# Performance work log

Hardware: AMD Instinct MI355X
Metric: run time of the kernel (lower is better)

Reference implementation:

```python
import jax, jax.numpy as jnp
import numpy as np

N = 50000       # nodes
E = 800000      # raw edges (self-loops added in reference, per PyG GATConv default)
F_IN = 256      # input feature dim (dataset.num_features stand-in)
H = 4           # heads (layer 1)
C = 32          # hidden_channels per head
CLS = 16        # num_classes (layer 2 out, heads=1)


def setup_inputs() -> dict:
    key = jax.random.key(0)
    ks = jax.random.split(key, 12)
    s = 0.05
    return {
        "x": jax.random.normal(ks[0], (N, F_IN), jnp.float32),
        "edge_index": jax.random.randint(ks[1], (2, E), 0, N, dtype=jnp.int64),
        "W1": jax.random.normal(ks[2], (F_IN, H * C), jnp.float32) * s,
        "att_src1": jax.random.normal(ks[3], (H, C), jnp.float32) * s,
        "att_dst1": jax.random.normal(ks[4], (H, C), jnp.float32) * s,
        "b1": jnp.zeros((H * C,), jnp.float32),
        "W2": jax.random.normal(ks[5], (H * C, CLS), jnp.float32) * s,
        "att_src2": jax.random.normal(ks[6], (1, CLS), jnp.float32) * s,
        "att_dst2": jax.random.normal(ks[7], (1, CLS), jnp.float32) * s,
        "b2": jnp.zeros((CLS,), jnp.float32),
    }


def gat_conv(x, src, dst, W, a_src, a_dst, b, heads, ch):
    """One GATConv (concat=True). src/dst include self-loops."""
    n = x.shape[0]
    h = (x @ W).reshape(n, heads, ch)                       # [N,H,C]
    alpha_s = jnp.sum(h * a_src, axis=-1)                   # [N,H]
    alpha_d = jnp.sum(h * a_dst, axis=-1)                   # [N,H]
    e = jax.nn.leaky_relu(alpha_s[src] + alpha_d[dst], 0.2) # [E',H]
    # segment softmax over incoming edges of each destination node
    m = jax.ops.segment_max(e, dst, num_segments=n)         # [N,H]
    ex = jnp.exp(e - m[dst])
    den = jax.ops.segment_sum(ex, dst, num_segments=n)      # [N,H]
    coef = ex / (den[dst] + 1e-16)                          # [E',H]
    # weighted scatter-aggregate of source features
    out = jax.ops.segment_sum(h[src] * coef[:, :, None], dst, num_segments=n)
    return out.reshape(n, heads * ch) + b


def reference(x, edge_index, W1, att_src1, att_dst1, b1, W2, att_src2, att_dst2, b2):
    n = x.shape[0]
    loop = jnp.arange(n, dtype=edge_index.dtype)
    src = jnp.concatenate([edge_index[0], loop])
    dst = jnp.concatenate([edge_index[1], loop])
    # eval mode: F.dropout is identity
    h = gat_conv(x, src, dst, W1, att_src1, att_dst1, b1, H, C)
    h = jax.nn.elu(h)
    out = gat_conv(h, src, dst, W2, att_src2, att_dst2, b2, 1, CLS)
    return out
```

## Files before the change

### kernel.cpp

```cpp
#include <hip/hip_runtime.h>
#include <hip/hip_bf16.h>
#include <math.h>

#define NNODES 50000
#define FIN 256
#define HH 4
#define CC 32
#define D1 128
#define CLS 16
#define NBUCK ((NNODES + 255) >> 8)
#define CHUNK 4096

typedef __attribute__((ext_vector_type(8))) short bfrag8;
typedef __attribute__((ext_vector_type(4))) float facc4;

__device__ __forceinline__ float lrelu(float x){ return x > 0.f ? x : 0.2f*x; }

__device__ __forceinline__ float fexp(float x){
#if __has_builtin(__builtin_amdgcn_exp2f)
  return __builtin_amdgcn_exp2f(x * 1.4426950408889634f);
#else
  return exp2f(x * 1.4426950408889634f);
#endif
}

__device__ __forceinline__ unsigned short f2bu(float x){
  __hip_bfloat16 h = __float2bfloat16(x);
  return *reinterpret_cast<unsigned short*>(&h);
}
__device__ __forceinline__ unsigned int pbf(float a, float b){
  return (unsigned int)f2bu(a) | ((unsigned int)f2bu(b) << 16);
}
__device__ __forceinline__ float2 bf2x(unsigned int u){
  float2 r;
  r.x = __uint_as_float(u << 16);
  r.y = __uint_as_float(u & 0xffff0000u);
  return r;
}

__global__ void wprep_kernel(const float* __restrict__ W, unsigned short* __restrict__ Wt) {
  int t = blockIdx.x*256 + threadIdx.x;
  if (t >= FIN*D1) return;
  int k = t >> 7, c = t & 127;
  Wt[c*FIN + k] = f2bu(W[t]);
}

__global__ __launch_bounds__(256) void gemm1_mfma(const float* __restrict__ x,
                                                  const unsigned int* __restrict__ Wt,
                                                  unsigned int* __restrict__ h1b) {
  __shared__ unsigned int Bs[128*256/2];
  __shared__ unsigned int As[64*64/2];
  int tid = threadIdx.x;
  int wv = tid >> 6, lane = tid & 63;
  int r0 = blockIdx.x * 64;

  for (int it = 0; it < 16; it++) {
    int w16 = it*256 + tid;
    int c = w16 >> 5, k8 = w16 & 31;
    uint4 v = ((const uint4*)Wt)[w16];
    int byt = (c*512 + k8*16) ^ ((c&7)<<4);
    *(uint4*)((char*)Bs + byt) = v;
  }

  facc4 acc[8];
  #pragma unroll
  for (int t=0;t<8;t++) acc[t] = (facc4){0.f,0.f,0.f,0.f};

  int arow = tid >> 2, apart = tid & 3;
  int mrow = lane & 15, kb = lane >> 4;

  for (int stage = 0; stage < 4; stage++) {
    int gr = r0 + arow;
    const float* src = x + (size_t)gr*FIN + stage*64 + apart*16;
    float4 f0, f1, f2, f3;
    if (gr < NNODES) {
      f0 = *(const float4*)(src);
      f1 = *(const float4*)(src+4);
      f2 = *(const float4*)(src+8);
      f3 = *(const float4*)(src+12);
    } else {
      f0 = f1 = f2 = f3 = make_float4(0.f,0.f,0.f,0.f);
    }
    uint4 u0, u1;
    u0.x = pbf(f0.x,f0.y); u0.y = pbf(f0.z,f0.w);
    u0.z = pbf(f1.x,f1.y); u0.w = pbf(f1.z,f1.w);
    u1.x = pbf(f2.x,f2.y); u1.y = pbf(f2.z,f2.w);
    u1.z = pbf(f3.x,f3.y); u1.w = pbf(f3.z,f3.w);
    __syncthreads();
    int b0 = (arow*128 + apart*32) ^ ((arow&7)<<4);
    int b1 = (arow*128 + apart*32 + 16) ^ ((arow&7)<<4);
    *(uint4*)((char*)As + b0) = u0;
    *(uint4*)((char*)As + b1) = u1;
    __syncthreads();
    #pragma unroll
    for (int ks = 0; ks < 2; ks++) {
      int row = wv*16 + mrow;
      int abyt = (row*128 + ks*64 + kb*16) ^ ((row&7)<<4);
      bfrag8 afrag = *(bfrag8*)((char*)As + abyt);
      #pragma unroll
      for (int ct = 0; ct < 8; ct++) {
        int c = ct*16 + mrow;
        int bbyt = (c*512 + stage*128 + ks*64 + kb*16) ^ ((c&7)<<4);
        bfrag8 bfrag = *(bfrag8*)((char*)Bs + bbyt);
        acc[ct] = __builtin_amdgcn_mfma_f32_16x16x32_bf16(afrag, bfrag, acc[ct], 0, 0, 0);
      }
    }
  }
  int orow0 = r0 + wv*16 + (lane>>4)*4;
  int ocol = lane & 15;
  #pragma unroll
  for (int r=0; r<4; r++) {
    int gr = orow0 + r;
    if (gr < NNODES) {
      #pragma unroll
      for (int ct=0; ct<4; ct++)
        h1b[(size_t)gr*64 + ct*16 + ocol] = pbf(acc[ct][r], acc[ct+4][r]);
    }
  }
}

__global__ void alpha1_kernel(const unsigned int* __restrict__ h1b,
                              const float* __restrict__ asrc,
                              const float* __restrict__ adst,
                              float* __restrict__ as1, float* __restrict__ ad1) {
  int t = blockIdx.x * blockDim.x + threadIdx.x;
  if (t >= NNODES*HH) return;
  int i = t >> 2, h = t & 3;
  const unsigned int* base = h1b + (size_t)i*64 + (h&1)*32;
  const float* ap = asrc + h*CC;
  const float* bp = adst + h*CC;
  bool hi = (h >= 2);
  float s=0.f, d=0.f;
  #pragma unroll
  for (int q8=0; q8<8; q8++){
    uint4 u = *(const uint4*)(base + q8*4);
    float v0 = hi ? bf2x(u.x).y : bf2x(u.x).x;
    float v1 = hi ? bf2x(u.y).y : bf2x(u.y).x;
    float v2 = hi ? bf2x(u.z).y : bf2x(u.z).x;
    float v3 = hi ? bf2x(u.w).y : bf2x(u.w).x;
    int q = q8*4;
    s = fmaf(v0, ap[q+0], s); d = fmaf(v0, bp[q+0], d);
    s = fmaf(v1, ap[q+1], s); d = fmaf(v1, bp[q+1], d);
    s = fmaf(v2, ap[q+2], s); d = fmaf(v2, bp[q+2], d);
    s = fmaf(v3, ap[q+3], s); d = fmaf(v3, bp[q+3], d);
  }
  as1[t] = s; ad1[t] = d;
}

__global__ __launch_bounds__(256) void bucket_count_kernel(const int* __restrict__ dsts,
                                                           int* __restrict__ bcnt, int E) {
  __shared__ int cnt[NBUCK];
  for (int t=threadIdx.x; t<NBUCK; t+=256) cnt[t]=0;
  __syncthreads();
  int base = blockIdx.x*CHUNK, lim = min(base+CHUNK, E);
  for (int e = base+threadIdx.x; e < lim; e += 256)
    atomicAdd(&cnt[dsts[e]>>8], 1);
  __syncthreads();
  for (int t=threadIdx.x; t<NBUCK; t+=256)
    if (cnt[t]) atomicAdd(&bcnt[t], cnt[t]);
}

__global__ __launch_bounds__(256) void bucket_scan_kernel(const int* __restrict__ bcnt,
                                                          int* __restrict__ gstart,
                                                          int* __restrict__ gcur) {
  int t = threadIdx.x;
  int orig = (t < NBUCK) ? bcnt[t] : 0;
  int v = orig;
  int ln = t & 63, wv = t >> 6;
  #pragma unroll
  for (int off=1; off<64; off<<=1){ int u=__shfl_up(v,off,64); if(ln>=off) v+=u; }
  __shared__ int wsum[4], wbase[4];
  if (ln==63) wsum[wv]=v;
  __syncthreads();
  if (t==0){
    int s=0;
    for(int k=0;k<4;k++){ wbase[k]=s; s+=wsum[k]; }
  }
  __syncthreads();
  int incl = wbase[wv]+v;
  if (t < NBUCK){ gstart[t+1]=incl; gcur[t]=incl-orig; }
  if (t==0) gstart[0]=0;
}

__global__ __launch_bounds__(256) void bin_kernel(const int* __restrict__ srcs,
                                                  const int* __restrict__ dsts,
                                                  int* __restrict__ gcur,
                                                  unsigned int* __restrict__ binned, int E) {
  __shared__ int cnt[NBUCK];
  __shared__ int rbase[NBUCK];
  for (int t=threadIdx.x; t<NBUCK; t+=256) cnt[t]=0;
  __syncthreads();
  int base = blockIdx.x*CHUNK, lim = min(base+CHUNK, E);
  for (int e = base+threadIdx.x; e < lim; e += 256)
    atomicAdd(&cnt[dsts[e]>>8], 1);
  __syncthreads();
  for (int t=threadIdx.x; t<NBUCK; t+=256){
    rbase[t] = cnt[t] ? atomicAdd(&gcur[t], cnt[t]) : 0;
    cnt[t] = 0;
  }
  __syncthreads();
  for (int e = base+threadIdx.x; e < lim; e += 256){
    int d = dsts[e], s = srcs[e];
    int b = d >> 8;
    int p = rbase[b] + atomicAdd(&cnt[b], 1);
    binned[p] = ((unsigned int)s << 8) | (unsigned int)(d & 255);
  }
}

__global__ __launch_bounds__(256) void bucketcsr_kernel(const int* __restrict__ gstart,
                                                        const unsigned int* __restrict__ binned,
                                                        int* __restrict__ offs,
                                                        unsigned short* __restrict__ srcsort, int E) {
  int b = blockIdx.x;
  int s0 = gstart[b], s1 = gstart[b+1];
  int t = threadIdx.x;
  __shared__ int cnt[256];
  __shared__ int cur[256];
  cnt[t] = 0;
  __syncthreads();
  for (int j = s0+t; j < s1; j += 256)
    atomicAdd(&cnt[binned[j] & 255], 1);
  __syncthreads();
  int orig = cnt[t], v = orig;
  int ln = t & 63, wv = t >> 6;
  #pragma unroll
  for (int off=1; off<64; off<<=1){ int u=__shfl_up(v,off,64); if(ln>=off) v+=u; }
  __shared__ int wsum[4], wbase[4];
  if (ln==63) wsum[wv]=v;
  __syncthreads();
  if (t==0){
    int s=0;
    for(int k=0;k<4;k++){ wbase[k]=s; s+=wsum[k]; }
  }
  __syncthreads();
  int excl = wbase[wv] + v - orig;
  cur[t] = excl;
  int node = b*256 + t;
  if (node < NNODES) offs[node] = s0 + excl;
  if (node == NNODES-1) offs[NNODES] = E;
  __syncthreads();
  for (int j = s0+t; j < s1; j += 256){
    unsigned int e = binned[j];
    int p = s0 + atomicAdd(&cur[e & 255], 1);
    srcsort[p] = (unsigned short)(e >> 8);
  }
}

__global__ __launch_bounds__(256) void agg1_kernel(
    const unsigned int* __restrict__ h1b, const float* __restrict__ as1,
    const float* __restrict__ ad1, const int* __restrict__ offs,
    const unsigned short* __restrict__ srcsort, const float* __restrict__ b1,
    unsigned int* __restrict__ out1p) {
  __shared__ float exs[4][4][64];
  __shared__ int   ss [4][64];
  int warp = threadIdx.x >> 6;
  int lane = threadIdx.x & 63;
  int i = blockIdx.x * 4 + warp;
  if (i >= NNODES) return;
  int start = offs[i], end = offs[i+1];
  float4 adv = *(const float4*)(ad1 + (size_t)i*4);
  float4 asv = *(const float4*)(as1 + (size_t)i*4);
  float ad[4] = {adv.x, adv.y, adv.z, adv.w};
  float wself[4];
  {
    float av[4] = {asv.x, asv.y, asv.z, asv.w};
    #pragma unroll
    for (int h=0;h<4;h++) wself[h] = fexp(lrelu(av[h] + ad[h]));
  }
  int hlo = lane >> 5, hhi = hlo + 2;
  float den[4] = {0.f, 0.f, 0.f, 0.f};
  float accA, accB;
  {
    float2 hv = bf2x(h1b[(size_t)i*64 + lane]);
    accA = wself[hlo] * hv.x; accB = wself[hhi] * hv.y;
  }
  for (int c0 = start; c0 < end; c0 += 64) {
    int cnt = min(64, end - c0);
    int j = c0 + lane;
    if (j < end) {
      int s = (int)srcsort[j];
      float4 a = *(const float4*)(as1 + (size_t)s*4);
      float e0 = fexp(lrelu(a.x + ad[0]));
      float e1 = fexp(lrelu(a.y + ad[1]));
      float e2 = fexp(lrelu(a.z + ad[2]));
      float e3 = fexp(lrelu(a.w + ad[3]));
      den[0] += e0; den[1] += e1; den[2] += e2; den[3] += e3;
      exs[warp][0][lane] = e0; exs[warp][1][lane] = e1;
      exs[warp][2][lane] = e2; exs[warp][3][lane] = e3;
      ss[warp][lane] = s;
    }
    #pragma unroll 8
    for (int j2 = 0; j2 < cnt; j2++) {
      int s = ss[warp][j2];
      float2 hv = bf2x(h1b[(size_t)s*64 + lane]);
      accA = fmaf(exs[warp][hlo][j2], hv.x, accA);
      accB = fmaf(exs[warp][hhi][j2], hv.y, accB);
    }
  }
  #pragma unroll
  for (int off=1; off<64; off<<=1) {
    #pragma unroll
    for (int h=0;h<4;h++) den[h] += __shfl_xor(den[h], off, 64);
  }
  float invlo = 1.f / (den[hlo] + wself[hlo] + 1e-16f);
  float invhi = 1.f / (den[hhi] + wself[hhi] + 1e-16f);
  float v0 = accA * invlo + b1[lane];
  float v1 = accB * invhi + b1[lane + 64];
  v0 = v0 > 0.f ? v0 : fexp(v0) - 1.f;
  v1 = v1 > 0.f ? v1 : fexp(v1) - 1.f;
  out1p[(size_t)i*64 + lane] = pbf(v0, v1);
}

__global__ __launch_bounds__(256) void layer2_proj_kernel(
    const unsigned int* __restrict__ out1p, const float* __restrict__ W2,
    const float* __restrict__ asrc2, const float* __restrict__ adst2,
    __hip_bfloat16* __restrict__ h2b, float* __restrict__ as2, float* __restrict__ ad2) {
  __shared__ float w_s[D1*CLS];
  for (int l = threadIdx.x; l < D1*CLS; l += 256) w_s[l] = W2[l];
  __syncthreads();
  int warp = threadIdx.x >> 6, lane = threadIdx.x & 63;
  int i = blockIdx.x*4 + warp;
  if (i >= NNODES) return;
  int c = lane & 15, kq = lane >> 4;
  const unsigned int* xp = out1p + (size_t)i*64 + (kq&1)*32;
  bool hi = kq >= 2;
  int kb = (kq&1)*32 + (hi ? 64 : 0);
  float acc = 0.f;
  #pragma unroll
  for (int q8=0; q8<8; q8++) {
    uint4 u = *(const uint4*)(xp + q8*4);
    float v0 = hi ? bf2x(u.x).y : bf2x(u.x).x;
    float v1 = hi ? bf2x(u.y).y : bf2x(u.y).x;
    float v2 = hi ? bf2x(u.z).y : bf2x(u.z).x;
    float v3 = hi ? bf2x(u.w).y : bf2x(u.w).x;
    int k = kb + q8*4;
    acc = fmaf(v0, w_s[(k+0)*CLS + c], acc);
    acc = fmaf(v1, w_s[(k+1)*CLS + c], acc);
    acc = fmaf(v2, w_s[(k+2)*CLS + c], acc);
    acc = fmaf(v3, w_s[(k+3)*CLS + c], acc);
  }
  acc += __shfl_xor(acc, 16, 64);
  acc += __shfl_xor(acc, 32, 64);
  if (lane < 16) h2b[(size_t)i*CLS + c] = __float2bfloat16(acc);
  float s = acc * asrc2[c];
  float d = acc * adst2[c];
  #pragma unroll
  for (int off=1; off<16; off<<=1) { s += __shfl_xor(s, off, 64); d += __shfl_xor(d, off, 64); }
  if (lane == 0) { as2[i] = s; ad2[i] = d; }
}

__global__ __launch_bounds__(256) void agg2_kernel(
    const unsigned int* __restrict__ h2b, const float* __restrict__ as2,
    const float* __restrict__ ad2, const int* __restrict__ offs,
    const unsigned short* __restrict__ srcsort, const float* __restrict__ b2,
    float* __restrict__ out) {
  int warp = threadIdx.x >> 6, lane = threadIdx.x & 63;
  int i = blockIdx.x*4 + warp;
  if (i >= NNODES) return;
  int start = offs[i], end = offs[i+1];
  float ad = ad2[i];
  float wself = fexp(lrelu(as2[i] + ad));
  int g = lane >> 3, cp = lane & 7;
  float2 acc = make_float2(0.f, 0.f);
  float denp = 0.f;
  if (g == 0) {
    float2 hv = bf2x(h2b[(size_t)i*(CLS/2) + cp]);
    acc.x = wself*hv.x; acc.y = wself*hv.y;
    denp = wself;
  }
  #pragma unroll 4
  for (int j = start + g; j < end; j += 8) {
    int s = (int)srcsort[j];
    float w = fexp(lrelu(as2[s] + ad));
    denp += w;
    float2 hv = bf2x(h2b[(size_t)s*(CLS/2) + cp]);
    acc.x = fmaf(w, hv.x, acc.x);
    acc.y = fmaf(w, hv.y, acc.y);
  }
  #pragma unroll
  for (int off=8; off<64; off<<=1) {
    acc.x += __shfl_xor(acc.x, off, 64);
    acc.y += __shfl_xor(acc.y, off, 64);
    denp  += __shfl_xor(denp,  off, 64);
  }
  if (lane < 8) {
    float inv = 1.f / (denp + 1e-16f);
    float2 o;
    o.x = acc.x * inv + b2[2*cp];
    o.y = acc.y * inv + b2[2*cp+1];
    *(float2*)(out + (size_t)i*CLS + 2*cp) = o;
  }
}

extern "C" void kernel_launch(void* const* d_in, const int* in_sizes, int n_in,
                              void* d_out, int out_size, void* d_ws, size_t ws_size,
                              hipStream_t stream) {
  const float* x     = (const float*)d_in[0];
  const int*   eidx  = (const int*)d_in[1];
  const float* W1    = (const float*)d_in[2];
  const float* asrc1 = (const float*)d_in[3];
  const float* adst1 = (const float*)d_in[4];
  const float* b1    = (const float*)d_in[5];
  const float* W2    = (const float*)d_in[6];
  const float* asrc2 = (const float*)d_in[7];
  const float* adst2 = (const float*)d_in[8];
  const float* b2    = (const float*)d_in[9];
  float* out = (float*)d_out;

  const int E = in_sizes[1] / 2;
  const int* srcs = eidx;
  const int* dsts = eidx + E;
  const int EBLK = (E + CHUNK - 1) / CHUNK;

  char* ws = (char*)d_ws;
  size_t off = 0;
  auto alloc = [&](size_t bytes) -> void* {
    void* p = ws + off;
    off = (off + bytes + 255) & ~(size_t)255;
    return p;
  };
  unsigned int*   h1b     = (unsigned int*)alloc((size_t)NNODES*(D1/2)*4);
  unsigned int*   out1p   = (unsigned int*)alloc((size_t)NNODES*(D1/2)*4);
  unsigned short* Wt      = (unsigned short*)alloc((size_t)FIN*D1*2);
  float*          as1     = (float*)alloc((size_t)NNODES*HH*4);
  float*          ad1     = (float*)alloc((size_t)NNODES*HH*4);
  __hip_bfloat16* h2b     = (__hip_bfloat16*)alloc((size_t)NNODES*CLS*2);
  float*          as2     = (float*)alloc((size_t)NNODES*4);
  float*          ad2     = (float*)alloc((size_t)NNODES*4);
  int*            bcnt    = (int*)alloc((size_t)NBUCK*4);
  int*            gstart  = (int*)alloc((size_t)(NBUCK+1)*4);
  int*            gcur    = (int*)alloc((size_t)NBUCK*4);
  int*            offs    = (int*)alloc((size_t)(NNODES+1)*4);
  unsigned int*   binned  = (unsigned int*)alloc((size_t)E*4);
  unsigned short* srcsort = (unsigned short*)alloc((size_t)E*2);

  (void)hipMemsetAsync(bcnt, 0, (size_t)NBUCK*4, stream);

  wprep_kernel<<<(FIN*D1+255)/256, 256, 0, stream>>>(W1, Wt);
  gemm1_mfma<<<(NNODES+63)/64, 256, 0, stream>>>(x, (const unsigned int*)Wt, h1b);
  alpha1_kernel<<<(NNODES*HH+255)/256, 256, 0, stream>>>(h1b, asrc1, adst1, as1, ad1);

  bucket_count_kernel<<<EBLK, 256, 0, stream>>>(dsts, bcnt, E);
  bucket_scan_kernel<<<1, 256, 0, stream>>>(bcnt, gstart, gcur);
  bin_kernel<<<EBLK, 256, 0, stream>>>(srcs, dsts, gcur, binned, E);
  bucketcsr_kernel<<<NBUCK, 256, 0, stream>>>(gstart, binned, offs, srcsort, E);

  agg1_kernel<<<(NNODES+3)/4, 256, 0, stream>>>(h1b, as1, ad1, offs, srcsort, b1, out1p);

  layer2_proj_kernel<<<(NNODES+3)/4, 256, 0, stream>>>(out1p, W2, asrc2, adst2, h2b, as2, ad2);
  agg2_kernel<<<(NNODES+3)/4, 256, 0, stream>>>((const unsigned int*)h2b, as2, ad2, offs, srcsort, b2, out);
}
```

Measured before the change: 158.5 us.

## Split wave into edge groups with wide vector gathers in both aggregation kernels

In layer-1 aggregation, each wave is split into 4 groups of 16 lanes. Each lane loads 16 bytes of the source node's bf16 features, so four edges are gathered at once instead of one edge per 64-lane row, and partial sums are then combined with cross-group shuffles. Layer-2 aggregation now stages edge weights and source indices in shared memory in 64-edge chunks, so the exp is computed once per edge rather than per lane group. It then gathers 16 edges at a time with 8-byte loads per lane. The aim is more memory-level parallelism and fewer, wider gather instructions, at the cost of extra shuffle reductions and more registers.

```diff
diff --git a/kernel.cpp b/kernel.cpp
--- a/kernel.cpp
+++ b/kernel.cpp
@@ -267,12 +267,18 @@
     #pragma unroll
     for (int h=0;h<4;h++) wself[h] = fexp(lrelu(av[h] + ad[h]));
   }
-  int hlo = lane >> 5, hhi = hlo + 2;
+  int cq = lane & 15, g = lane >> 4;
+  int hlo = cq >> 3, hhi = hlo + 2;
   float den[4] = {0.f, 0.f, 0.f, 0.f};
-  float accA, accB;
-  {
-    float2 hv = bf2x(h1b[(size_t)i*64 + lane]);
-    accA = wself[hlo] * hv.x; accB = wself[hhi] * hv.y;
+  float accL[4] = {0.f,0.f,0.f,0.f}, accH[4] = {0.f,0.f,0.f,0.f};
+  if (g == 0) {
+    uint4 u = *(const uint4*)(h1b + (size_t)i*64 + 4*cq);
+    float wl = wself[hlo], wh = wself[hhi];
+    float2 p0 = bf2x(u.x), p1 = bf2x(u.y), p2 = bf2x(u.z), p3 = bf2x(u.w);
+    accL[0] = wl*p0.x; accH[0] = wh*p0.y;
+    accL[1] = wl*p1.x; accH[1] = wh*p1.y;
+    accL[2] = wl*p2.x; accH[2] = wh*p2.y;
+    accL[3] = wl*p3.x; accH[3] = wh*p3.y;
   }
   for (int c0 = start; c0 < end; c0 += 64) {
     int cnt = min(64, end - c0);
@@ -289,12 +295,25 @@
       exs[warp][2][lane] = e2; exs[warp][3][lane] = e3;
       ss[warp][lane] = s;
     }
-    #pragma unroll 8
-    for (int j2 = 0; j2 < cnt; j2++) {
+    #pragma unroll 4
+    for (int j2 = g; j2 < cnt; j2 += 4) {
       int s = ss[warp][j2];
-      float2 hv = bf2x(h1b[(size_t)s*64 + lane]);
-      accA = fmaf(exs[warp][hlo][j2], hv.x, accA);
-      accB = fmaf(exs[warp][hhi][j2], hv.y, accB);
+      float wl = exs[warp][hlo][j2];
+      float wh = exs[warp][hhi][j2];
+      uint4 u = *(const uint4*)(h1b + (size_t)s*64 + 4*cq);
+      float2 p0 = bf2x(u.x), p1 = bf2x(u.y), p2 = bf2x(u.z), p3 = bf2x(u.w);
+      accL[0] = fmaf(wl, p0.x, accL[0]); accH[0] = fmaf(wh, p0.y, accH[0]);
+      accL[1] = fmaf(wl, p1.x, accL[1]); accH[1] = fmaf(wh, p1.y, accH[1]);
+      accL[2] = fmaf(wl, p2.x, accL[2]); accH[2] = fmaf(wh, p2.y, accH[2]);
+      accL[3] = fmaf(wl, p3.x, accL[3]); accH[3] = fmaf(wh, p3.y, accH[3]);
+    }
+  }
+  #pragma unroll
+  for (int off=16; off<64; off<<=1) {
+    #pragma unroll
+    for (int k=0;k<4;k++) {
+      accL[k] += __shfl_xor(accL[k], off, 64);
+      accH[k] += __shfl_xor(accH[k], off, 64);
     }
   }
   #pragma unroll
@@ -302,13 +321,26 @@
     #pragma unroll
     for (int h=0;h<4;h++) den[h] += __shfl_xor(den[h], off, 64);
   }
-  float invlo = 1.f / (den[hlo] + wself[hlo] + 1e-16f);
-  float invhi = 1.f / (den[hhi] + wself[hhi] + 1e-16f);
-  float v0 = accA * invlo + b1[lane];
-  float v1 = accB * invhi + b1[lane + 64];
-  v0 = v0 > 0.f ? v0 : fexp(v0) - 1.f;
-  v1 = v1 > 0.f ? v1 : fexp(v1) - 1.f;
-  out1p[(size_t)i*64 + lane] = pbf(v0, v1);
+  if (g == 0) {
+    float invlo = 1.f / (den[hlo] + wself[hlo] + 1e-16f);
+    float invhi = 1.f / (den[hhi] + wself[hhi] + 1e-16f);
+    float4 bL = *(const float4*)(b1 + 4*cq);
+    float4 bH = *(const float4*)(b1 + 64 + 4*cq);
+    float vL[4], vH[4];
+    vL[0]=accL[0]*invlo+bL.x; vL[1]=accL[1]*invlo+bL.y;
+    vL[2]=accL[2]*invlo+bL.z; vL[3]=accL[3]*invlo+bL.w;
+    vH[0]=accH[0]*invhi+bH.x; vH[1]=accH[1]*invhi+bH.y;
+    vH[2]=accH[2]*invhi+bH.z; vH[3]=accH[3]*invhi+bH.w;
+    #pragma unroll
+    for (int k=0;k<4;k++){
+      vL[k] = vL[k] > 0.f ? vL[k] : fexp(vL[k]) - 1.f;
+      vH[k] = vH[k] > 0.f ? vH[k] : fexp(vH[k]) - 1.f;
+    }
+    uint4 o;
+    o.x = pbf(vL[0], vH[0]); o.y = pbf(vL[1], vH[1]);
+    o.z = pbf(vL[2], vH[2]); o.w = pbf(vL[3], vH[3]);
+    *(uint4*)(out1p + (size_t)i*64 + 4*cq) = o;
+  }
 }
 
 __global__ __launch_bounds__(256) void layer2_proj_kernel(
@@ -354,41 +386,59 @@
     const float* __restrict__ ad2, const int* __restrict__ offs,
     const unsigned short* __restrict__ srcsort, const float* __restrict__ b2,
     float* __restrict__ out) {
+  __shared__ float wls[4][64];
+  __shared__ int   ss2[4][64];
   int warp = threadIdx.x >> 6, lane = threadIdx.x & 63;
   int i = blockIdx.x*4 + warp;
   if (i >= NNODES) return;
   int start = offs[i], end = offs[i+1];
   float ad = ad2[i];
   float wself = fexp(lrelu(as2[i] + ad));
-  int g = lane >> 3, cp = lane & 7;
-  float2 acc = make_float2(0.f, 0.f);
+  int c2 = lane & 3, g = lane >> 2;
+  float acc[4] = {0.f,0.f,0.f,0.f};
   float denp = 0.f;
   if (g == 0) {
-    float2 hv = bf2x(h2b[(size_t)i*(CLS/2) + cp]);
-    acc.x = wself*hv.x; acc.y = wself*hv.y;
-    denp = wself;
-  }
-  #pragma unroll 4
-  for (int j = start + g; j < end; j += 8) {
-    int s = (int)srcsort[j];
-    float w = fexp(lrelu(as2[s] + ad));
-    denp += w;
-    float2 hv = bf2x(h2b[(size_t)s*(CLS/2) + cp]);
-    acc.x = fmaf(w, hv.x, acc.x);
-    acc.y = fmaf(w, hv.y, acc.y);
-  }
-  #pragma unroll
-  for (int off=8; off<64; off<<=1) {
-    acc.x += __shfl_xor(acc.x, off, 64);
-    acc.y += __shfl_xor(acc.y, off, 64);
-    denp  += __shfl_xor(denp,  off, 64);
-  }
-  if (lane < 8) {
+    uint2 u = *(const uint2*)(h2b + (size_t)i*8 + 2*c2);
+    float2 p0 = bf2x(u.x), p1 = bf2x(u.y);
+    acc[0] = wself*p0.x; acc[1] = wself*p0.y;
+    acc[2] = wself*p1.x; acc[3] = wself*p1.y;
+  }
+  if (lane == 0) denp = wself;
+  for (int c0 = start; c0 < end; c0 += 64) {
+    int cnt = min(64, end - c0);
+    int j = c0 + lane;
+    if (j < end) {
+      int s = (int)srcsort[j];
+      float w = fexp(lrelu(as2[s] + ad));
+      denp += w;
+      wls[warp][lane] = w;
+      ss2[warp][lane] = s;
+    }
+    #pragma unroll 4
+    for (int j2 = g; j2 < cnt; j2 += 16) {
+      int s = ss2[warp][j2];
+      float w = wls[warp][j2];
+      uint2 u = *(const uint2*)(h2b + (size_t)s*8 + 2*c2);
+      float2 p0 = bf2x(u.x), p1 = bf2x(u.y);
+      acc[0] = fmaf(w, p0.x, acc[0]); acc[1] = fmaf(w, p0.y, acc[1]);
+      acc[2] = fmaf(w, p1.x, acc[2]); acc[3] = fmaf(w, p1.y, acc[3]);
+    }
+  }
+  #pragma unroll
+  for (int off=4; off<64; off<<=1) {
+    #pragma unroll
+    for (int k=0;k<4;k++) acc[k] += __shfl_xor(acc[k], off, 64);
+  }
+  #pragma unroll
+  for (int off=1; off<64; off<<=1) denp += __shfl_xor(denp, off, 64);
+  if (g == 0) {
     float inv = 1.f / (denp + 1e-16f);
-    float2 o;
-    o.x = acc.x * inv + b2[2*cp];
-    o.y = acc.y * inv + b2[2*cp+1];
-    *(float2*)(out + (size_t)i*CLS + 2*cp) = o;
+    float4 o;
+    o.x = acc[0]*inv + b2[4*c2+0];
+    o.y = acc[1]*inv + b2[4*c2+1];
+    o.z = acc[2]*inv + b2[4*c2+2];
+    o.w = acc[3]*inv + b2[4*c2+3];
+    *(float4*)(out + (size_t)i*CLS + 4*c2) = o;
   }
 }
 
```

New measurement: 168.8 us. 6.5% more time.
